# Kernel tuning notes

Hardware: AMD Instinct MI355X
Metric: run time of the kernel (lower is better)

## Reference

```python
import jax, jax.numpy as jnp
import numpy as np

N, V, O, H = 8192, 8, 16, 128
STEP = 2.0  # TRAJECTORY_PIONTS_LENGTH
DIST_COST, OBST_COST, OBST_RADIUS = 1.0, 0.1, 1.0
VEH_COST, VEH_RADIUS = 0.1, 1.0


def setup_inputs() -> dict:
    key = jax.random.key(0)
    k1, k2 = jax.random.split(key)
    prediction = jax.random.normal(k1, (N, V, H, 1), dtype=jnp.float32)
    inputs = jax.random.normal(k2, (N, 4 * V + 3 * O), dtype=jnp.float32)
    return {"prediction": prediction, "inputs": inputs}


def _masked_mean_inv(d, mask):
    # mean(1/d[mask]) if any, else 0 (matches torch's conditional add)
    cnt = jnp.sum(mask)
    inv = jnp.where(mask, 1.0 / jnp.where(mask, d, 1.0), 0.0)
    return jnp.where(cnt > 0, jnp.sum(inv) / jnp.maximum(cnt, 1).astype(d.dtype), 0.0)


def reference(prediction, inputs):
    vehicle_data = inputs[:, : 4 * V].reshape(N, V, 4)
    obstacle_data = inputs[:, 4 * V :].reshape(N, O, 3)
    vehicles = vehicle_data[:, :, :2]      # (N,V,2)
    target = vehicle_data[:, :, 2:]        # (N,V,2)
    obstacles = obstacle_data               # (N,O,3)

    # unit direction per step, then cumulative sum replaces the horizon loop
    step = jnp.concatenate((jnp.cos(prediction), jnp.sin(prediction)), axis=-1)  # (N,V,H,2)
    traj = vehicles[:, :, None, :] + jnp.cumsum(step * STEP, axis=2)             # (N,V,H,2)

    loss = jnp.mean(jnp.linalg.norm(target[:, :, None, :] - traj, axis=-1)) * DIST_COST

    # obstacle term: (N,V,O,H) pairwise distances, masked harmonic mean
    od = jnp.linalg.norm(traj[:, :, None, :, :] - obstacles[:, None, :, None, :2], axis=-1)
    omask = od < obstacles[:, None, :, None, 2] + OBST_RADIUS
    loss = loss + _masked_mean_inv(od, omask) * OBST_COST

    # vehicle-vehicle (adjacent index) proximity term: (N,V-1,H)
    vd = jnp.linalg.norm(traj[:, 1:, :, :] - traj[:, :-1, :, :], axis=-1)
    vmask = vd < VEH_RADIUS
    loss = loss + _masked_mean_inv(vd, vmask) * VEH_COST
    return loss
```

## Files before the change

kernel.cpp:

```cpp
#include <hip/hip_runtime.h>

namespace {
constexpr int kN = 8192, kV = 8, kO = 16, kH = 128;
constexpr float kStep = 2.0f;
constexpr float kDistCost = 1.0f, kObstCost = 0.1f, kObstRadius = 1.0f;
constexpr float kVehCost = 0.1f, kVehRadius = 1.0f;
constexpr int kInRow = 4 * kV + 3 * kO;
constexpr float kInv2Pi = 0.15915494309189535f;
}

typedef float v2f __attribute__((ext_vector_type(2)));

__device__ __forceinline__ float rfl_f(float x) {
  return __int_as_float(__builtin_amdgcn_readfirstlane(__float_as_int(x)));
}

template <int Ctrl, int RowMask, bool Bctrl>
__device__ __forceinline__ float dpp_mov0(float x) {
  return __int_as_float(__builtin_amdgcn_update_dpp(
      0, __float_as_int(x), Ctrl, RowMask, 0xf, Bctrl));
}

__device__ __forceinline__ float wave_incl_scan(float x) {
  x += dpp_mov0<0x111, 0xf, true>(x);
  x += dpp_mov0<0x112, 0xf, true>(x);
  x += dpp_mov0<0x114, 0xf, true>(x);
  x += dpp_mov0<0x118, 0xf, true>(x);
  x += dpp_mov0<0x142, 0xa, false>(x);
  x += dpp_mov0<0x143, 0xc, false>(x);
  return x;
}

__global__ __launch_bounds__(512) void loss_main(
    const float* __restrict__ pred, const float* __restrict__ inputs,
    float* __restrict__ partials) {
  const int n = blockIdx.x;
  const int tid = threadIdx.x;
  const int lane = tid & 63;
  const int v = __builtin_amdgcn_readfirstlane(tid >> 6);

  const float* __restrict__ row = inputs + (size_t)n * kInRow;

  __shared__ float4 sh_traj[kV * 64];
  __shared__ float sh_red[kV][5];

  float ox[kO], oy[kO], rr2[kO];
#pragma unroll
  for (int o = 0; o < kO; ++o) {
    ox[o] = rfl_f(row[4 * kV + 3 * o + 0]);
    oy[o] = rfl_f(row[4 * kV + 3 * o + 1]);
    float rr = row[4 * kV + 3 * o + 2] + kObstRadius;
    rr2[o] = rfl_f(rr > 0.f ? rr * rr : -1.0f);
  }
  const float vx = rfl_f(row[4 * v + 0]);
  const float vy = rfl_f(row[4 * v + 1]);
  const float tx = rfl_f(row[4 * v + 2]);
  const float ty = rfl_f(row[4 * v + 3]);

  const float2 th = ((const float2*)(pred + (size_t)n * (kV * kH)))[tid];
  v2f r01 = {th.x, th.y};
  r01 *= kInv2Pi;
  float c0 = __builtin_amdgcn_cosf(r01.x);
  float s0 = __builtin_amdgcn_sinf(r01.x);
  float c1 = __builtin_amdgcn_cosf(r01.y);
  float s1w = __builtin_amdgcn_sinf(r01.y);
  v2f step1 = {c1, s1w};
  step1 *= kStep;

  float Sx = wave_incl_scan((c0 + c1) * kStep);
  float Sy = wave_incl_scan((s0 + s1w) * kStep);
  const float px1 = vx + Sx, py1 = vy + Sy;
  const float px0 = px1 - step1.x, py0 = py1 - step1.y;

  sh_traj[v * 64 + lane] = make_float4(px0, py0, px1, py1);

  const v2f pxp = {px0, px1};
  const v2f pyp = {py0, py1};

  {
    v2f dx = tx - pxp;
    v2f dy = ty - pyp;
    v2f d2 = __builtin_elementwise_fma(dy, dy, dx * dx);
    v2f sq = {__builtin_amdgcn_sqrtf(d2.x), __builtin_amdgcn_sqrtf(d2.y)};
    sh_red[0][0] = 0.f;
    (void)sq;
  }
  v2f t_dx = tx - pxp;
  v2f t_dy = ty - pyp;
  v2f t_d2 = __builtin_elementwise_fma(t_dy, t_dy, t_dx * t_dx);
  float s1 = __builtin_amdgcn_sqrtf(t_d2.x) + __builtin_amdgcn_sqrtf(t_d2.y);

  v2f s2p = {0.f, 0.f};
  int c2i = 0;
#pragma unroll
  for (int o = 0; o < kO; ++o) {
    v2f dx = pxp - ox[o];
    v2f dy = pyp - oy[o];
    v2f d2 = __builtin_elementwise_fma(dy, dy, dx * dx);
    bool ma = d2.x < rr2[o];
    bool mb = d2.y < rr2[o];
    unsigned long long ba = __ballot(ma);
    unsigned long long bb = __ballot(mb);
    if (ba | bb) {
      float inva = __builtin_amdgcn_rsqf(d2.x);
      float invb = __builtin_amdgcn_rsqf(d2.y);
      v2f add = {ma ? inva : 0.f, mb ? invb : 0.f};
      s2p += add;
      c2i += (int)__popcll(ba) + (int)__popcll(bb);
    }
  }
  float s2 = s2p.x + s2p.y;

  __syncthreads();

  float s3 = 0.f;
  int c3i = 0;
  if (v < kV - 1) {
    float4 t2 = sh_traj[(v + 1) * 64 + lane];
    v2f ex = {t2.x, t2.z};
    v2f ey = {t2.y, t2.w};
    ex -= pxp;
    ey -= pyp;
    v2f e2 = __builtin_elementwise_fma(ey, ey, ex * ex);
    bool m0 = e2.x < kVehRadius * kVehRadius;
    bool m1 = e2.y < kVehRadius * kVehRadius;
    unsigned long long b0 = __ballot(m0);
    unsigned long long b1 = __ballot(m1);
    if (b0 | b1) {
      float i0 = __builtin_amdgcn_rsqf(e2.x);
      float i1 = __builtin_amdgcn_rsqf(e2.y);
      s3 = (m0 ? i0 : 0.f) + (m1 ? i1 : 0.f);
      c3i = (int)__popcll(b0) + (int)__popcll(b1);
    }
  }

  float r1s = wave_incl_scan(s1);
  float r2s = wave_incl_scan(s2);
  float r3s = wave_incl_scan(s3);
  if (lane == 63) {
    sh_red[v][0] = r1s;
    sh_red[v][1] = r2s;
    sh_red[v][2] = r3s;
    sh_red[v][3] = (float)c2i;
    sh_red[v][4] = (float)c3i;
  }
  __syncthreads();
  if (tid < 5) {
    float acc = 0.f;
#pragma unroll
    for (int w = 0; w < kV; ++w) acc += sh_red[w][tid];
    partials[tid * kN + n] = acc;
  }
}

__global__ __launch_bounds__(1024) void loss_final(
    const float* __restrict__ partials, float* __restrict__ out) {
  const int tid = threadIdx.x;
  const int lane = tid & 63;
  const int wave = tid >> 6;
  __shared__ float sh[16][5];
  float acc[5];
#pragma unroll
  for (int a = 0; a < 5; ++a) {
    const float4* pa = (const float4*)(partials + a * kN);
    float4 u = pa[tid];
    float4 w = pa[tid + 1024];
    acc[a] = (u.x + u.y) + (u.z + u.w) + (w.x + w.y) + (w.z + w.w);
  }
#pragma unroll
  for (int a = 0; a < 5; ++a) acc[a] = wave_incl_scan(acc[a]);
  if (lane == 63) {
#pragma unroll
    for (int a = 0; a < 5; ++a) sh[wave][a] = acc[a];
  }
  __syncthreads();
  if (tid == 0) {
    float t[5];
#pragma unroll
    for (int a = 0; a < 5; ++a) {
      float s = 0.f;
#pragma unroll
      for (int w = 0; w < 16; ++w) s += sh[w][a];
      t[a] = s;
    }
    float loss = t[0] * (1.0f / (float)(kN * kV * kH)) * kDistCost;
    if (t[3] > 0.f) loss += (t[1] / t[3]) * kObstCost;
    if (t[4] > 0.f) loss += (t[2] / t[4]) * kVehCost;
    out[0] = loss;
  }
}

extern "C" void kernel_launch(void* const* d_in, const int* in_sizes, int n_in,
                              void* d_out, int out_size, void* d_ws, size_t ws_size,
                              hipStream_t stream) {
  const float* pred = (const float*)d_in[0];
  const float* inputs = (const float*)d_in[1];
  float* partials = (float*)d_ws;
  loss_main<<<kN, 512, 0, stream>>>(pred, inputs, partials);
  loss_final<<<1, 1024, 0, stream>>>(partials, (float*)d_out);
}
```

Before: 105.4 us.

## Regroup obstacle test by time chunk and cull waves with bounding radius

Moves the obstacle-distance loop after the barrier and reassigns work so that each wave checks one block of 8 time steps across all 8 vehicles, read from shared memory. A per-row bounding radius (largest obstacle centre distance from the origin plus its radius, padded slightly) lets a whole wave skip the 16-obstacle loop when none of its points can be inside any obstacle. Grouping by time step clusters far-away late-trajectory points into the same waves, so more waves can skip. It also pads the shared trajectory array to avoid bank conflicts and drops a dead computation block. The cost is an extra shared-memory read and a per-thread square root loop over obstacles to build the radius.

Result: no change. 106.8 us (+1.4%).

```diff
diff --git a/kernel.cpp b/kernel.cpp
--- a/kernel.cpp
+++ b/kernel.cpp
@@ -37,21 +37,28 @@
   const int n = blockIdx.x;
   const int tid = threadIdx.x;
   const int lane = tid & 63;
-  const int v = __builtin_amdgcn_readfirstlane(tid >> 6);
+  const int w = __builtin_amdgcn_readfirstlane(tid >> 6);
+  const int v = w;
 
   const float* __restrict__ row = inputs + (size_t)n * kInRow;
 
-  __shared__ float4 sh_traj[kV * 64];
+  __shared__ float4 sh_p[kV * 65];
   __shared__ float sh_red[kV][5];
 
   float ox[kO], oy[kO], rr2[kO];
+  float R = 0.f;
 #pragma unroll
   for (int o = 0; o < kO; ++o) {
     ox[o] = rfl_f(row[4 * kV + 3 * o + 0]);
     oy[o] = rfl_f(row[4 * kV + 3 * o + 1]);
     float rr = row[4 * kV + 3 * o + 2] + kObstRadius;
     rr2[o] = rfl_f(rr > 0.f ? rr * rr : -1.0f);
-  }
+    float co = __builtin_amdgcn_sqrtf(fmaf(oy[o], oy[o], ox[o] * ox[o]));
+    R = fmaxf(R, rr > 0.f ? co + rr : 0.f);
+  }
+  R *= 1.0009765625f;
+  const float R2 = rfl_f(R * R);
+
   const float vx = rfl_f(row[4 * v + 0]);
   const float vy = rfl_f(row[4 * v + 1]);
   const float tx = rfl_f(row[4 * v + 2]);
@@ -72,51 +79,22 @@
   const float px1 = vx + Sx, py1 = vy + Sy;
   const float px0 = px1 - step1.x, py0 = py1 - step1.y;
 
-  sh_traj[v * 64 + lane] = make_float4(px0, py0, px1, py1);
+  sh_p[v * 65 + lane] = make_float4(px0, py0, px1, py1);
 
   const v2f pxp = {px0, px1};
   const v2f pyp = {py0, py1};
 
-  {
-    v2f dx = tx - pxp;
-    v2f dy = ty - pyp;
-    v2f d2 = __builtin_elementwise_fma(dy, dy, dx * dx);
-    v2f sq = {__builtin_amdgcn_sqrtf(d2.x), __builtin_amdgcn_sqrtf(d2.y)};
-    sh_red[0][0] = 0.f;
-    (void)sq;
-  }
   v2f t_dx = tx - pxp;
   v2f t_dy = ty - pyp;
   v2f t_d2 = __builtin_elementwise_fma(t_dy, t_dy, t_dx * t_dx);
   float s1 = __builtin_amdgcn_sqrtf(t_d2.x) + __builtin_amdgcn_sqrtf(t_d2.y);
 
-  v2f s2p = {0.f, 0.f};
-  int c2i = 0;
-#pragma unroll
-  for (int o = 0; o < kO; ++o) {
-    v2f dx = pxp - ox[o];
-    v2f dy = pyp - oy[o];
-    v2f d2 = __builtin_elementwise_fma(dy, dy, dx * dx);
-    bool ma = d2.x < rr2[o];
-    bool mb = d2.y < rr2[o];
-    unsigned long long ba = __ballot(ma);
-    unsigned long long bb = __ballot(mb);
-    if (ba | bb) {
-      float inva = __builtin_amdgcn_rsqf(d2.x);
-      float invb = __builtin_amdgcn_rsqf(d2.y);
-      v2f add = {ma ? inva : 0.f, mb ? invb : 0.f};
-      s2p += add;
-      c2i += (int)__popcll(ba) + (int)__popcll(bb);
-    }
-  }
-  float s2 = s2p.x + s2p.y;
-
   __syncthreads();
 
   float s3 = 0.f;
   int c3i = 0;
   if (v < kV - 1) {
-    float4 t2 = sh_traj[(v + 1) * 64 + lane];
+    float4 t2 = sh_p[(v + 1) * 65 + lane];
     v2f ex = {t2.x, t2.z};
     v2f ey = {t2.y, t2.w};
     ex -= pxp;
@@ -134,21 +112,49 @@
     }
   }
 
+  const int v2i = lane >> 3;
+  const int j = lane & 7;
+  float4 q = sh_p[v2i * 65 + w * 8 + j];
+  const v2f qx = {q.x, q.z};
+  const v2f qy = {q.y, q.w};
+  float s2 = 0.f;
+  int c2i = 0;
+  v2f q2 = __builtin_elementwise_fma(qy, qy, qx * qx);
+  bool near = (q2.x < R2) || (q2.y < R2);
+  if (__ballot(near)) {
+#pragma unroll
+    for (int o = 0; o < kO; ++o) {
+      v2f dx = qx - ox[o];
+      v2f dy = qy - oy[o];
+      v2f d2 = __builtin_elementwise_fma(dy, dy, dx * dx);
+      bool ma = d2.x < rr2[o];
+      bool mb = d2.y < rr2[o];
+      unsigned long long ba = __ballot(ma);
+      unsigned long long bb = __ballot(mb);
+      if (ba | bb) {
+        float inva = __builtin_amdgcn_rsqf(d2.x);
+        float invb = __builtin_amdgcn_rsqf(d2.y);
+        s2 += (ma ? inva : 0.f) + (mb ? invb : 0.f);
+        c2i += (int)__popcll(ba) + (int)__popcll(bb);
+      }
+    }
+  }
+
   float r1s = wave_incl_scan(s1);
   float r2s = wave_incl_scan(s2);
   float r3s = wave_incl_scan(s3);
   if (lane == 63) {
-    sh_red[v][0] = r1s;
-    sh_red[v][1] = r2s;
-    sh_red[v][2] = r3s;
-    sh_red[v][3] = (float)c2i;
-    sh_red[v][4] = (float)c3i;
+    sh_red[w][0] = r1s;
+    sh_red[w][1] = r2s;
+    sh_red[w][2] = r3s;
+    sh_red[w][3] = (float)c2i;
+    sh_red[w][4] = (float)c3i;
   }
   __syncthreads();
   if (tid < 5) {
     float acc = 0.f;
 #pragma unroll
-    for (int w = 0; w < kV; ++w) acc += sh_red[w][tid];
+    for (int k = 0; k < kV; ++k) acc += sh_red[k][tid];
     partials[tid * kN + n] = acc;
   }
 }
@@ -180,7 +186,7 @@
     for (int a = 0; a < 5; ++a) {
       float s = 0.f;
 #pragma unroll
-      for (int w = 0; w < 16; ++w) s += sh[w][a];
+      for (int k = 0; k < 16; ++k) s += sh[k][a];
       t[a] = s;
     }
     float loss = t[0] * (1.0f / (float)(kN * kV * kH)) * kDistCost;
```
